# Performance work log

Measured on AMD Instinct MI355X. Metric: run time of the kernel, lower is better.

## Reference

```python
import jax, jax.numpy as jnp
import numpy as np

# AAA hyperparameters (init_kwargs)
ALPHA = 1.0
TAU = 6.0
KAPPA = 100
T_TEMP = 1.0
BETA = 5.0
LR = 0.1
# torch.optim.AdamW defaults
B1, B2, EPS, WD = 0.9, 0.999, 1e-8, 0.01

B, D, C = 4096, 2048, 1000


def setup_inputs() -> dict:
    key = jax.random.key(0)
    kx, kw, kb = jax.random.split(key, 3)
    x = jax.random.normal(kx, (B, D), dtype=jnp.float32)
    W = jax.random.normal(kw, (D, C), dtype=jnp.float32) * 0.02  # linear classifier weight
    b = jax.random.normal(kb, (C,), dtype=jnp.float32) * 0.01
    return {"x": x, "W": W, "b": b}


def _ce(logits, y):
    # per-sample cross-entropy (nn.CrossEntropyLoss(reduce=False))
    return jax.nn.logsumexp(logits, axis=1) - jnp.take_along_axis(logits, y[:, None], axis=1)[:, 0]


def reference(x, W, b):
    # model inference under torch.no_grad(); z is detached in AAA
    z = jax.lax.stop_gradient(x @ W + b)  # [B, C]
    y = jnp.argmax(z, axis=1)             # pred_y, constant indices

    l_org = _ce(z, y)                                            # [B]
    l_atr = (jnp.floor(l_org / TAU) + 0.5) * TAU                 # [B]
    # AAA_type == 'sin'
    l_trg = l_org - ALPHA * TAU * jnp.sin(jnp.pi * (1.0 - 2.0 * (l_org - l_atr) / TAU))
    p_trg = jnp.max(jax.nn.softmax(z / T_TEMP, axis=1), axis=1)  # [B]

    def loss_fn(u):
        term1 = jnp.abs(_ce(u, y) - l_trg)                       # [B]
        # NOTE: torch.max(F.softmax(u, dim=1)) has NO dim arg -> GLOBAL max scalar,
        # broadcast against p_trg [B]. Faithful to the source.
        term2 = BETA * jnp.abs(jnp.max(jax.nn.softmax(u, axis=1)) - p_trg)
        return jnp.sum(term1 + term2)

    grad_fn = jax.grad(loss_fn)

    def adamw_step(carry, t):
        u, m, v = carry
        g = grad_fn(u)
        u = u * (1.0 - LR * WD)                  # decoupled weight decay (torch AdamW)
        m = B1 * m + (1.0 - B1) * g
        v = B2 * v + (1.0 - B2) * g * g
        mhat = m / (1.0 - jnp.power(B1, t))
        vhat = v / (1.0 - jnp.power(B2, t))
        u = u - LR * mhat / (jnp.sqrt(vhat) + EPS)
        return (u, m, v), None

    init = (z, jnp.zeros_like(z), jnp.zeros_like(z))
    steps = jnp.arange(1, KAPPA + 1, dtype=jnp.float32)
    (u, _, _), _ = jax.lax.scan(adamw_step, init, steps)
    return u  # protected logits [B, C]
```

## Files before the change

kernel.cpp:

```cpp
#include <hip/hip_runtime.h>

#define BB 4096
#define DD 2048
#define CC 1000

__device__ __forceinline__ float fexp(float x) { return __expf(x); }
__device__ __forceinline__ float flog(float x) { return __logf(x); }
__device__ __forceinline__ float frcp(float x) {
  return __builtin_amdgcn_rcpf(x);
}
__device__ __forceinline__ float fsqrt(float x) {
  return __builtin_amdgcn_sqrtf(x);
}

__device__ __forceinline__ void wave_argmax(float& val, int& idx) {
#pragma unroll
  for (int off = 1; off < 64; off <<= 1) {
    float ov = __shfl_xor(val, off, 64);
    int oi = __shfl_xor(idx, off, 64);
    if (ov > val || (ov == val && oi < idx)) { val = ov; idx = oi; }
  }
}

__device__ __forceinline__ float wave_sum(float v) {
#pragma unroll
  for (int off = 1; off < 64; off <<= 1) v += __shfl_xor(v, off, 64);
  return v;
}

__global__ __launch_bounds__(256) void gemm_kernel(
    const float* __restrict__ X, const float* __restrict__ W,
    const float* __restrict__ Bv, float* __restrict__ Z) {
  __shared__ float sA[16][68];
  __shared__ float sB[16][68];
  const int tid = threadIdx.x;
  const int rowTile = blockIdx.y * 64;
  const int colTile = blockIdx.x * 64;
  const int tx = tid & 15, ty = tid >> 4;
  float acc[4][4] = {};

  const int aRow = tid >> 2;
  const int aK = (tid & 3) << 2;
  const int bK = tid >> 4;
  const int bC = (tid & 15) << 2;
  const bool fullCol = (colTile + 64) <= CC;

  for (int k0 = 0; k0 < DD; k0 += 16) {
    const float4 av = *(const float4*)&X[(size_t)(rowTile + aRow) * DD + k0 + aK];
    sA[aK + 0][aRow] = av.x;
    sA[aK + 1][aRow] = av.y;
    sA[aK + 2][aRow] = av.z;
    sA[aK + 3][aRow] = av.w;
    float4 bv;
    if (fullCol) {
      bv = *(const float4*)&W[(size_t)(k0 + bK) * CC + colTile + bC];
    } else {
      const int c0 = colTile + bC;
      bv.x = (c0 + 0 < CC) ? W[(size_t)(k0 + bK) * CC + c0 + 0] : 0.f;
      bv.y = (c0 + 1 < CC) ? W[(size_t)(k0 + bK) * CC + c0 + 1] : 0.f;
      bv.z = (c0 + 2 < CC) ? W[(size_t)(k0 + bK) * CC + c0 + 2] : 0.f;
      bv.w = (c0 + 3 < CC) ? W[(size_t)(k0 + bK) * CC + c0 + 3] : 0.f;
    }
    *(float4*)&sB[bK][bC] = bv;
    __syncthreads();
#pragma unroll
    for (int kk = 0; kk < 16; ++kk) {
      const float4 a4 = *(const float4*)&sA[kk][ty << 2];
      const float4 b4 = *(const float4*)&sB[kk][tx << 2];
      const float ar[4] = {a4.x, a4.y, a4.z, a4.w};
      const float br[4] = {b4.x, b4.y, b4.z, b4.w};
#pragma unroll
      for (int i = 0; i < 4; ++i)
#pragma unroll
        for (int j = 0; j < 4; ++j) acc[i][j] = fmaf(ar[i], br[j], acc[i][j]);
    }
    __syncthreads();
  }
#pragma unroll
  for (int i = 0; i < 4; ++i) {
    const int r = rowTile + (ty << 2) + i;
#pragma unroll
    for (int j = 0; j < 4; ++j) {
      const int c = colTile + (tx << 2) + j;
      if (c < CC) Z[(size_t)r * CC + c] = acc[i][j] + Bv[c];
    }
  }
}

__global__ __launch_bounds__(256) void stats_kernel(
    const float* __restrict__ Z, int* __restrict__ Y,
    float* __restrict__ Lt, float* __restrict__ Pt) {
  const int wave = threadIdx.x >> 6, lane = threadIdx.x & 63;
  const int row = blockIdx.x * 4 + wave;
  float uv[16];
#pragma unroll
  for (int k = 0; k < 16; ++k) {
    const int j = lane + (k << 6);
    uv[k] = (j < CC) ? Z[(size_t)row * CC + j] : -__builtin_inff();
  }
  float mx = uv[0];
  int ai = lane;
#pragma unroll
  for (int k = 1; k < 16; ++k) {
    const int j = lane + (k << 6);
    if (uv[k] > mx) { mx = uv[k]; ai = j; }
  }
  wave_argmax(mx, ai);
  float sum = 0.f;
#pragma unroll
  for (int k = 0; k < 16; ++k) sum += fexp(uv[k] - mx);
  sum = wave_sum(sum);
  if (lane == 0) {
    const float lse = mx + flog(sum);
    const float lorg = lse - mx;
    const float latr = (floorf(lorg / 6.0f) + 0.5f) * 6.0f;
    const float lt =
        lorg - 6.0f * sinf(3.14159265358979323846f *
                           (1.0f - 2.0f * (lorg - latr) / 6.0f));
    Y[row] = ai;
    Lt[row] = lt;
    Pt[row] = frcp(sum);
  }
}

__global__ __launch_bounds__(1024) void sort_kernel(
    const float* __restrict__ P, float* __restrict__ Out) {
  __shared__ float s[4096];
  const int tid = threadIdx.x;
  for (int i = tid; i < 4096; i += 1024) s[i] = P[i];
  __syncthreads();
  for (int k = 2; k <= 4096; k <<= 1) {
    for (int j = k >> 1; j > 0; j >>= 1) {
      for (int i = tid; i < 4096; i += 1024) {
        const int ixj = i ^ j;
        if (ixj > i) {
          const float a = s[i], b = s[ixj];
          const bool up = ((i & k) == 0);
          if (up ? (a > b) : (a < b)) { s[i] = b; s[ixj] = a; }
        }
      }
      __syncthreads();
    }
  }
  for (int i = tid; i < 4096; i += 1024) Out[i] = s[i];
}

__global__ __launch_bounds__(1024, 1) void opt_kernel(
    float* __restrict__ ZU, const int* __restrict__ Yarr,
    const float* __restrict__ Ltrg, const float* __restrict__ Sorted,
    unsigned long long* __restrict__ Slots) {
  const int tid = threadIdx.x;
  const int wave = tid >> 6, lane = tid & 63;
  const int row = blockIdx.x * 16 + wave;

  __shared__ float s_sorted[4096];
  __shared__ float s_coarse[64];
  __shared__ float s_cval[2][16];
  __shared__ int s_cidx[2][16];
  __shared__ float s_coef[2];
  __shared__ int s_rc[2];
  __shared__ int s_arrive[2];
  __shared__ int s_done[2];

  for (int i = tid; i < 4096; i += 1024) s_sorted[i] = Sorted[i];
  if (tid < 64) s_coarse[tid] = Sorted[tid << 6];
  if (tid == 0) {
    s_arrive[0] = 0;
    s_arrive[1] = 0;
    s_done[0] = 0;
    s_done[1] = 0;
  }

  float u[16], m[16], v[16], e[16];
#pragma unroll
  for (int k = 0; k < 16; ++k) {
    const int j = lane + (k << 6);
    u[k] = (j < CC) ? ZU[(size_t)row * CC + j] : -__builtin_inff();
    m[k] = 0.f;
    v[k] = 0.f;
  }
  const int y = Yarr[row];
  const float ltrg = Ltrg[row];
  const int ky = y >> 6, ly = y & 63;

  float pb1 = 1.0f, pb2 = 1.0f;
  __syncthreads();

#pragma unroll 1
  for (int t = 1; t <= 100; ++t) {
    const int p = t & 1;
    pb1 *= 0.9f;
    pb2 *= 0.999f;
    const float im1 = frcp(1.0f - pb1);
    const float im2 = frcp(1.0f - pb2);

    float mx = u[0];
    int ai = lane;
#pragma unroll
    for (int k = 1; k < 16; ++k) {
      const int j = lane + (k << 6);
      if (u[k] > mx) { mx = u[k]; ai = j; }
    }
    wave_argmax(mx, ai);
    float sum = 0.f;
#pragma unroll
    for (int k = 0; k < 16; ++k) {
      e[k] = fexp(u[k] - mx);
      sum += e[k];
    }
    sum = wave_sum(sum);
    const float lse = mx + flog(sum);
    float uyl = 0.f;
#pragma unroll
    for (int k = 0; k < 16; ++k) uyl = (k == ky) ? u[k] : uyl;
    const float uy = __shfl(uyl, ly, 64);
    const float ce = lse - uy;
    const float pmax = frcp(sum);
    const float a = (ce > ltrg) ? 1.0f : ((ce < ltrg) ? -1.0f : 0.0f);

    if (lane == 0) {
      s_cval[p][wave] = pmax;
      s_cidx[p][wave] = (row << 10) | ai;
      __hip_atomic_fetch_add(&s_arrive[p], 1, __ATOMIC_RELEASE,
                             __HIP_MEMORY_SCOPE_WORKGROUP);
    }
    const int target = 16 * ((t >> 1) + (t & 1));
    while (__hip_atomic_load(&s_arrive[p], __ATOMIC_ACQUIRE,
                             __HIP_MEMORY_SCOPE_WORKGROUP) < target) {
    }

    float bv = s_cval[p][0];
    int bi = s_cidx[p][0];
#pragma unroll
    for (int w = 1; w < 16; ++w) {
      const float ov = s_cval[p][w];
      const int oi = s_cidx[p][w];
      if (ov > bv || (ov == bv && oi < bi)) { bv = ov; bi = oi; }
    }
    const int candw = (bi >> 10) & 15;
    const bool iscand = (wave == candw);

    unsigned long long* slot_buf = &Slots[p * 256];
    if (tid == 0) {
      const unsigned long long pack =
          ((unsigned long long)__float_as_uint(bv) << 32) |
          (unsigned)((t << 24) | bi);
      __hip_atomic_store(&slot_buf[blockIdx.x], pack, __ATOMIC_RELAXED,
                         __HIP_MEMORY_SCOPE_AGENT);
    }

    auto adam_update = [&](bool with_t2, float coef, int cstar) {
#pragma unroll
      for (int k = 0; k < 16; ++k) {
        const int j = lane + (k << 6);
        const float p2 = e[k] * pmax;
        float g = a * (p2 - ((j == y) ? 1.0f : 0.0f));
        if (with_t2) g += coef * (((j == cstar) ? 1.0f : 0.0f) - p2);
        u[k] *= 0.999f;
        m[k] = 0.9f * m[k] + 0.1f * g;
        v[k] = 0.999f * v[k] + 0.001f * g * g;
        const float mh = m[k] * im1;
        const float vh = v[k] * im2;
        u[k] -= 0.1f * mh * frcp(fsqrt(vh) + 1e-8f);
      }
    };

    if (!iscand && wave != 0) adam_update(false, 0.f, 0);

    if (wave == 0) {
      if (!iscand) adam_update(false, 0.f, 0);
      unsigned long long pv[4];
      unsigned fresh = 0u;
      while (fresh != 0xFu) {
#pragma unroll
        for (int q = 0; q < 4; ++q) {
          if (!(fresh & (1u << q))) {
            const unsigned long long pk = __hip_atomic_load(
                &slot_buf[lane + (q << 6)], __ATOMIC_RELAXED,
                __HIP_MEMORY_SCOPE_AGENT);
            if ((unsigned)((pk >> 24) & 0xFFu) == (unsigned)t) {
              pv[q] = pk;
              fresh |= 1u << q;
            }
          }
        }
        if (fresh != 0xFu) __builtin_amdgcn_s_sleep(1);
      }
      float gv = -1.0f;
      int gi = 0x7fffffff;
#pragma unroll
      for (int q = 0; q < 4; ++q) {
        const float ov = __uint_as_float((unsigned)(pv[q] >> 32));
        const int oi = (int)(pv[q] & 0x3FFFFFu);
        if (ov > gv || (ov == gv && oi < gi)) { gv = ov; gi = oi; }
      }
      wave_argmax(gv, gi);
      const float ss = gv;
      const float v1 = s_coarse[lane];
      const int c1 = __popcll(__ballot(v1 < ss));
      int nlt = 0;
      if (c1 > 0) {
        const float v2 = s_sorted[((c1 - 1) << 6) + lane];
        nlt = ((c1 - 1) << 6) + __popcll(__ballot(v2 < ss));
      }
      const int c2 = __popcll(__ballot(v1 <= ss));
      int nle = 0;
      if (c2 > 0) {
        const float v3 = s_sorted[((c2 - 1) << 6) + lane];
        nle = ((c2 - 1) << 6) + __popcll(__ballot(v3 <= ss));
      }
      const int S = nlt - (4096 - nle);
      if (lane == 0) {
        s_coef[p] = 5.0f * (float)S * ss;
        s_rc[p] = gi;
        __hip_atomic_store(&s_done[p], t, __ATOMIC_RELEASE,
                           __HIP_MEMORY_SCOPE_WORKGROUP);
      }
    }

    if (iscand) {
      while (__hip_atomic_load(&s_done[p], __ATOMIC_ACQUIRE,
                               __HIP_MEMORY_SCOPE_WORKGROUP) < t) {
      }
      const int rc = s_rc[p];
      const bool win = ((rc >> 10) == row);
      adam_update(win, s_coef[p], rc & 1023);
    }
  }

#pragma unroll
  for (int k = 0; k < 16; ++k) {
    const int j = lane + (k << 6);
    if (j < CC) ZU[(size_t)row * CC + j] = u[k];
  }
}

extern "C" void kernel_launch(void* const* d_in, const int* in_sizes, int n_in,
                              void* d_out, int out_size, void* d_ws,
                              size_t ws_size, hipStream_t stream) {
  const float* x = (const float*)d_in[0];
  const float* W = (const float*)d_in[1];
  const float* b = (const float*)d_in[2];
  float* z = (float*)d_out;

  char* ws = (char*)d_ws;
  int* y_arr = (int*)ws;
  float* ltrg_arr = (float*)(ws + (16 << 10));
  float* ptrg_arr = (float*)(ws + (32 << 10));
  float* sorted = (float*)(ws + (48 << 10));
  unsigned long long* slots =
      (unsigned long long*)(ws + (64 << 10));

  gemm_kernel<<<dim3(16, 64), 256, 0, stream>>>(x, W, b, z);
  stats_kernel<<<dim3(1024), 256, 0, stream>>>(z, y_arr, ltrg_arr, ptrg_arr);
  sort_kernel<<<dim3(1), 1024, 0, stream>>>(ptrg_arr, sorted);

  void* args[5] = {&z, &y_arr, &ltrg_arr, &sorted, &slots};
  hipLaunchCooperativeKernel((const void*)opt_kernel, dim3(256), dim3(1024),
                             args, 0u, stream);
}
```

Baseline: 1.124 ms.

## Replace FP32 SIMT GEMM with split-bf16 three-pass MFMA GEMM

Inputs are split into high and low bf16 halves, and the weight matrix is transposed, in two conversion kernels. A new MFMA kernel then computes the logits as hi*hi + lo*hi + hi*lo, which approximates FP32 accuracy on matrix cores instead of scalar FMAs. This costs extra conversion passes, about 44MB of workspace, and some precision loss that could change argmax ties downstream. The new path only runs when the workspace is large enough, otherwise the old GEMM is used.

```diff
diff --git a/kernel.cpp b/kernel.cpp
--- a/kernel.cpp
+++ b/kernel.cpp
@@ -3,6 +3,18 @@
 #define BB 4096
 #define DD 2048
 #define CC 1000
+
+typedef short short8 __attribute__((ext_vector_type(8)));
+typedef float f32x4 __attribute__((ext_vector_type(4)));
+
+__device__ __forceinline__ unsigned short f2bf(float x) {
+  unsigned u = __float_as_uint(x);
+  unsigned r = (u + 0x7FFFu + ((u >> 16) & 1u)) >> 16;
+  return (unsigned short)r;
+}
+__device__ __forceinline__ float bf2f(unsigned short h) {
+  return __uint_as_float(((unsigned)h) << 16);
+}
 
 __device__ __forceinline__ float fexp(float x) { return __expf(x); }
 __device__ __forceinline__ float flog(float x) { return __logf(x); }
@@ -38,13 +50,9 @@
   const int colTile = blockIdx.x * 64;
   const int tx = tid & 15, ty = tid >> 4;
   float acc[4][4] = {};
-
-  const int aRow = tid >> 2;
-  const int aK = (tid & 3) << 2;
-  const int bK = tid >> 4;
-  const int bC = (tid & 15) << 2;
+  const int aRow = tid >> 2, aK = (tid & 3) << 2;
+  const int bK = tid >> 4, bC = (tid & 15) << 2;
   const bool fullCol = (colTile + 64) <= CC;
-
   for (int k0 = 0; k0 < DD; k0 += 16) {
     const float4 av = *(const float4*)&X[(size_t)(rowTile + aRow) * DD + k0 + aK];
     sA[aK + 0][aRow] = av.x;
@@ -87,6 +95,156 @@
   }
 }
 
+__global__ __launch_bounds__(256) void conv_a(
+    const float* __restrict__ A, unsigned short* __restrict__ Ah,
+    unsigned short* __restrict__ Al) {
+  const int i = (blockIdx.x * 256 + threadIdx.x) * 4;
+  const float4 v = *(const float4*)(A + i);
+  ushort4 h, l;
+  h.x = f2bf(v.x); l.x = f2bf(v.x - bf2f(h.x));
+  h.y = f2bf(v.y); l.y = f2bf(v.y - bf2f(h.y));
+  h.z = f2bf(v.z); l.z = f2bf(v.z - bf2f(h.z));
+  h.w = f2bf(v.w); l.w = f2bf(v.w - bf2f(h.w));
+  *(ushort4*)(Ah + i) = h;
+  *(ushort4*)(Al + i) = l;
+}
+
+__global__ __launch_bounds__(256) void conv_b(
+    const float* __restrict__ B, unsigned short* __restrict__ Bht,
+    unsigned short* __restrict__ Blt) {
+  __shared__ float t[32][33];
+  const int kt = blockIdx.x * 32;
+  const int nt = blockIdx.y * 32;
+  const int tx = threadIdx.x & 31, ty = threadIdx.x >> 5;
+#pragma unroll
+  for (int r = 0; r < 4; ++r) {
+    const int k = kt + ty + r * 8, n = nt + tx;
+    t[ty + r * 8][tx] = (n < CC) ? B[(size_t)k * CC + n] : 0.f;
+  }
+  __syncthreads();
+#pragma unroll
+  for (int r = 0; r < 4; ++r) {
+    const int n = nt + ty + r * 8, k = kt + tx;
+    if (n < CC) {
+      const float v = t[tx][ty + r * 8];
+      const unsigned short h = f2bf(v);
+      Bht[(size_t)n * DD + k] = h;
+      Blt[(size_t)n * DD + k] = f2bf(v - bf2f(h));
+    }
+  }
+}
+
+#define PITCH 68
+__global__ __launch_bounds__(256) void mfma_gemm(
+    const unsigned short* __restrict__ Ah, const unsigned short* __restrict__ Al,
+    const unsigned short* __restrict__ Bht, const unsigned short* __restrict__ Blt,
+    const float* __restrict__ Bv, float* __restrict__ Z) {
+  __shared__ unsigned short sA[128 * PITCH];
+  __shared__ unsigned short sB[128 * PITCH];
+  const int tid = threadIdx.x;
+  const int n0 = blockIdx.x * 128;
+  const int m0 = blockIdx.y * 128;
+  const int wave = tid >> 6, lane = tid & 63;
+  const int wr = (wave >> 1) * 64;
+  const int wc = (wave & 1) * 64;
+  const int fr = lane & 15;
+  const int fq = lane >> 4;
+
+  f32x4 acc[4][4] = {};
+
+  const int sr = tid >> 1;
+  const int sc = (tid & 1) * 32;
+  const bool bvalid = (n0 + sr) < CC;
+
+  union Frag {
+    short8 v;
+    uint2 u[2];
+  };
+
+  for (int s = 0; s < 96; ++s) {
+    const int kp = s << 6;
+    const int seg = kp >> 11;
+    const int kk = kp & 2047;
+    const unsigned short* Asrc = (seg == 1) ? Al : Ah;
+    const unsigned short* Bsrc = (seg == 2) ? Blt : Bht;
+
+    uint4 av0, av1, av2, av3, bv0, bv1, bv2, bv3;
+    {
+      const uint4* gA =
+          (const uint4*)(Asrc + (size_t)(m0 + sr) * DD + kk + sc);
+      av0 = gA[0]; av1 = gA[1]; av2 = gA[2]; av3 = gA[3];
+      if (bvalid) {
+        const uint4* gB =
+            (const uint4*)(Bsrc + (size_t)(n0 + sr) * DD + kk + sc);
+        bv0 = gB[0]; bv1 = gB[1]; bv2 = gB[2]; bv3 = gB[3];
+      } else {
+        bv0 = bv1 = bv2 = bv3 = make_uint4(0, 0, 0, 0);
+      }
+    }
+    __syncthreads();
+    {
+      unsigned short* dA = sA + sr * PITCH + sc;
+      ((uint2*)(dA + 0))[0] = make_uint2(av0.x, av0.y);
+      ((uint2*)(dA + 4))[0] = make_uint2(av0.z, av0.w);
+      ((uint2*)(dA + 8))[0] = make_uint2(av1.x, av1.y);
+      ((uint2*)(dA + 12))[0] = make_uint2(av1.z, av1.w);
+      ((uint2*)(dA + 16))[0] = make_uint2(av2.x, av2.y);
+      ((uint2*)(dA + 20))[0] = make_uint2(av2.z, av2.w);
+      ((uint2*)(dA + 24))[0] = make_uint2(av3.x, av3.y);
+      ((uint2*)(dA + 28))[0] = make_uint2(av3.z, av3.w);
+      unsigned short* dB = sB + sr * PITCH + sc;
+      ((uint2*)(dB + 0))[0] = make_uint2(bv0.x, bv0.y);
+      ((uint2*)(dB + 4))[0] = make_uint2(bv0.z, bv0.w);
+      ((uint2*)(dB + 8))[0] = make_uint2(bv1.x, bv1.y);
+      ((uint2*)(dB + 12))[0] = make_uint2(bv1.z, bv1.w);
+      ((uint2*)(dB + 16))[0] = make_uint2(bv2.x, bv2.y);
+      ((uint2*)(dB + 20))[0] = make_uint2(bv2.z, bv2.w);
+      ((uint2*)(dB + 24))[0] = make_uint2(bv3.x, bv3.y);
+      ((uint2*)(dB + 28))[0] = make_uint2(bv3.z, bv3.w);
+    }
+    __syncthreads();
+
+#pragma unroll
+    for (int h = 0; h < 2; ++h) {
+      const int ko = h * 32 + fq * 8;
+      Frag a4[4], b4[4];
+#pragma unroll
+      for (int mt = 0; mt < 4; ++mt) {
+        const unsigned short* p = sA + (wr + mt * 16 + fr) * PITCH + ko;
+        a4[mt].u[0] = *(const uint2*)(p);
+        a4[mt].u[1] = *(const uint2*)(p + 4);
+      }
+#pragma unroll
+      for (int nt = 0; nt < 4; ++nt) {
+        const unsigned short* p = sB + (wc + nt * 16 + fr) * PITCH + ko;
+        b4[nt].u[0] = *(const uint2*)(p);
+        b4[nt].u[1] = *(const uint2*)(p + 4);
+      }
+#pragma unroll
+      for (int mt = 0; mt < 4; ++mt)
+#pragma unroll
+        for (int nt = 0; nt < 4; ++nt)
+          acc[mt][nt] = __builtin_amdgcn_mfma_f32_16x16x32_bf16(
+              a4[mt].v, b4[nt].v, acc[mt][nt], 0, 0, 0);
+    }
+  }
+
+#pragma unroll
+  for (int nt = 0; nt < 4; ++nt) {
+    const int col = n0 + wc + nt * 16 + fr;
+    if (col < CC) {
+      const float bb = Bv[col];
+#pragma unroll
+      for (int mt = 0; mt < 4; ++mt) {
+        const int rbase = m0 + wr + mt * 16 + fq * 4;
+#pragma unroll
+        for (int r = 0; r < 4; ++r)
+          Z[(size_t)(rbase + r) * CC + col] = acc[mt][nt][r] + bb;
+      }
+    }
+  }
+}
+
 __global__ __launch_bounds__(256) void stats_kernel(
     const float* __restrict__ Z, int* __restrict__ Y,
     float* __restrict__ Lt, float* __restrict__ Pt) {
@@ -351,7 +509,22 @@
   unsigned long long* slots =
       (unsigned long long*)(ws + (64 << 10));
 
-  gemm_kernel<<<dim3(16, 64), 256, 0, stream>>>(x, W, b, z);
+  const size_t A_BYTES = (size_t)BB * DD * 2;
+  const size_t B_BYTES = (size_t)CC * DD * 2;
+  unsigned short* AhP = (unsigned short*)(ws + (1 << 20));
+  unsigned short* AlP = (unsigned short*)(ws + (1 << 20) + A_BYTES);
+  unsigned short* BhP = (unsigned short*)(ws + (1 << 20) + 2 * A_BYTES);
+  unsigned short* BlP =
+      (unsigned short*)(ws + (1 << 20) + 2 * A_BYTES + B_BYTES);
+  const bool use_mfma = ws_size >= ((size_t)44 << 20);
+
+  if (use_mfma) {
+    conv_a<<<dim3(8192), 256, 0, stream>>>(x, AhP, AlP);
+    conv_b<<<dim3(64, 32), 256, 0, stream>>>(W, BhP, BlP);
+    mfma_gemm<<<dim3(8, 32), 256, 0, stream>>>(AhP, AlP, BhP, BlP, b, z);
+  } else {
+    gemm_kernel<<<dim3(16, 64), 256, 0, stream>>>(x, W, b, z);
+  }
   stats_kernel<<<dim3(1024), 256, 0, stream>>>(z, y_arr, ltrg_arr, ptrg_arr);
   sort_kernel<<<dim3(1), 1024, 0, stream>>>(ptrg_arr, sorted);
 
```

Result: faster. 1.015 ms (-9.8%).
